# Performance work log

Measured on AMD Instinct MI355X. Metric: run time of the kernel, lower is better.

The kernel has to match this reference:

```python
import jax, jax.numpy as jnp
import numpy as np

LAG = 24      # lag (months of 20 days) in the train window
STEP = 20     # days per rebalancing step
ANNUAL = 252.0


def setup_inputs() -> dict:
    key = jax.random.key(0)
    Y = jax.random.normal(key, (20480, 128), dtype=jnp.float32) * 0.01  # daily returns
    a = jnp.full((1,), 0.997, dtype=jnp.float32)                        # EWMA decay param
    logridge = jnp.full((1,), float(np.log(1e-5)), dtype=jnp.float32)   # log ridge param
    return {"Y": Y, "a": a, "logridge": logridge}


def reference(Y, a, logridge):
    n, p = Y.shape
    W = n // STEP - LAG            # number of rolling windows (1000)
    T = LAG * STEP                 # train window length (480)
    a0 = a[0]
    ridge = jnp.exp(logridge[0])

    # EWMA weights: w_t = a^(T-1-t) (most recent day has weight 1), normalized to sum T
    expo = jnp.arange(T - 1, -1, -1, dtype=Y.dtype)
    w = a0 ** expo
    w = w / w.sum() * T
    wsum = w.sum()
    denom = 1.0 - (w * w).sum() / (T * T)   # bias correction (w**2 / T**2).sum()
    ones_p = jnp.ones((p,), Y.dtype)

    def per_window(j):
        # train: Y[(i-lag)*20 : i*20] with i = j + LAG  ->  rows [j*20, j*20+T)
        Yt = jax.lax.dynamic_slice(Y, (j * STEP, 0), (T, p))
        # test: Y[i*20 : (i+1)*20]
        Yte = jax.lax.dynamic_slice(Y, ((j + LAG) * STEP, 0), (STEP, p))
        mean = (w[:, None] * Yt).sum(axis=0) / wsum          # [p]
        Yc = Yt - mean[None, :]                               # [T, p]
        Sigma = (Yc.T @ (w[:, None] * Yc)) / T / denom        # [p, p] weighted covariance
        lam, U = jnp.linalg.eigh(Sigma)
        Pmat = (U / (ridge + lam)[None, :]) @ U.T             # ridge-shrunk precision
        # GMV weights: P @ 1 / (1' P 1)
        v = Pmat @ ones_p
        wgt = v / (ones_p @ v)
        ret = Yte @ wgt                                       # [STEP] portfolio returns
        e = ret.sum()                                         # cumulative test return
        s = (ret * ret).mean()                                # realized daily variance
        return e, s

    e_all, s_all = jax.vmap(per_window)(jnp.arange(W))
    vol = jnp.sqrt(s_all.mean() * ANNUAL)
    mu = e_all.mean() / STEP * ANNUAL
    sharpe = mu / vol
    return vol, mu, sharpe
```

## Files before the change

kernel.cpp:

```cpp
#include <hip/hip_runtime.h>
#include <math.h>

#define P 128
#define T_WIN 480
#define STEPD 20
#define LAG_W 24
#define NITER 12
#define SEG 64
#define PACK 8448
#define PCHUNK 33

__device__ __forceinline__ int tri_off(int r) {
  const int a = r >> 2, b = r & 3;
  return ((a + 1) * (2 * a + b)) << 2;
}

__device__ __forceinline__ void ewma_consts(float af, double& la, float& Sf, float& denomf) {
  const double a = (double)af;
  la = log(a);
  const double A480 = exp(480.0 * la);
  const double S = (1.0 - A480) / (1.0 - a);
  const double Su2 = (1.0 - A480 * A480) / (1.0 - a * a);
  Sf = (float)S;
  denomf = (float)(1.0 - Su2 / (S * S));
}

__global__ __launch_bounds__(256) void cblocks_kernel(const float* __restrict__ Y,
                                                      const float* __restrict__ aarg,
                                                      float* __restrict__ cvec,
                                                      float* __restrict__ Call, int K) {
  const int k = blockIdx.x;
  const int tid = threadIdx.x;
  const int ti = tid >> 4, tj = tid & 15;
  __shared__ float st[STEPD][P];
  __shared__ float sbwsm[STEPD];
  if (tid < STEPD) {
    const double la = log((double)aarg[0]);
    sbwsm[tid] = (float)exp(0.5 * (double)(STEPD - 1 - tid) * la);
  }
  __syncthreads();
  const float* __restrict__ Yb = Y + (size_t)k * STEPD * P;
  for (int i = tid; i < STEPD * P / 4; i += 256) {
    float4 v = ((const float4*)Yb)[i];
    const float sw = sbwsm[i >> 5];
    v.x *= sw; v.y *= sw; v.z *= sw; v.w *= sw;
    ((float4*)&st[0][0])[i] = v;
  }
  __syncthreads();

  float acc[8][8];
#pragma unroll
  for (int u = 0; u < 8; ++u)
#pragma unroll
    for (int v = 0; v < 8; ++v) acc[u][v] = 0.0f;

#pragma unroll 4
  for (int t = 0; t < STEPD; ++t) {
    float af[8], bf[8];
    *(float4*)(af)     = *(const float4*)&st[t][ti * 4];
    *(float4*)(af + 4) = *(const float4*)&st[t][64 + ti * 4];
    *(float4*)(bf)     = *(const float4*)&st[t][tj * 4];
    *(float4*)(bf + 4) = *(const float4*)&st[t][64 + tj * 4];
#pragma unroll
    for (int u = 0; u < 8; ++u)
#pragma unroll
      for (int v = 0; v < 8; ++v) acc[u][v] += af[u] * bf[v];
  }

  float* __restrict__ Ck = Call + (size_t)k * PACK;
#pragma unroll
  for (int u = 0; u < 8; ++u) {
    const int r = (u < 4) ? (ti * 4 + u) : (64 + ti * 4 + u - 4);
    const int offr = tri_off(r);
    if (tj * 4 <= r) {
      float4 o0;
      o0.x = acc[u][0]; o0.y = acc[u][1]; o0.z = acc[u][2]; o0.w = acc[u][3];
      *(float4*)(Ck + offr + tj * 4) = o0;
    }
    if (64 + tj * 4 <= r) {
      float4 o1;
      o1.x = acc[u][4]; o1.y = acc[u][5]; o1.z = acc[u][6]; o1.w = acc[u][7];
      *(float4*)(Ck + offr + 64 + tj * 4) = o1;
    }
  }
  if (tid < P) {
    float s = 0.0f;
    for (int t = 0; t < STEPD; ++t) s += sbwsm[t] * st[t][tid];
    cvec[(size_t)k * P + tid] = s;
  }
}

__global__ __launch_bounds__(256) void scan_kernel(float* __restrict__ Call,
                                                   const float* __restrict__ aarg) {
  __shared__ float asm_[SEG];
  const int tid = threadIdx.x;
  const int seg = blockIdx.x / PCHUNK;
  const int chunk = blockIdx.x - seg * PCHUNK;
  if (tid < SEG) {
    const double la = log((double)aarg[0]);
    asm_[tid] = (float)exp(-(double)(20 * tid) * la);
  }
  __syncthreads();
  const int e = chunk * 256 + tid;
  float* __restrict__ base = Call + ((size_t)seg * SEG) * PACK + e;
  float g = 0.0f;
#pragma unroll 4
  for (int k = 0; k < SEG; ++k) {
    const float c = base[(size_t)k * PACK];
    g = fmaf(asm_[k], c, g);
    base[(size_t)k * PACK] = g;
  }
}

__global__ __launch_bounds__(128, 2) void window14_kernel(
    const float* __restrict__ Y, const float* __restrict__ aarg,
    const float* __restrict__ logridge, const float* __restrict__ cvec,
    const float* __restrict__ Gall, float* __restrict__ e_all,
    float* __restrict__ s_all, int W) {
  const int bid = blockIdx.x;
  const int q = W >> 3, r8 = W & 7;
  const int xcd = bid & 7, idx = bid >> 3;
  const int j = ((xcd < r8) ? (xcd * (q + 1)) : (r8 * (q + 1) + (xcd - r8) * q)) + idx;

  const int tid = threadIdx.x;
  const int ti = tid >> 4, tj = tid & 15;
  const int lane = tid & 63;
  const int wv = tid >> 6;
  const int rowbase = ti * 16;

  __shared__ float Gsm[PACK];
  __shared__ float rsm[P];
  __shared__ float vsm[P];
  __shared__ float meansm[P];
  __shared__ float coefsm[LAG_W];
  __shared__ float2 gd_wave[2];
  __shared__ float rs_wave[2];
  __shared__ float retd[STEPD];

  double la_d;
  float S, denom;
  ewma_consts(aarg[0], la_d, S, denom);
  const float ridge = expf(logridge[0]);

  if (tid < LAG_W)
    coefsm[tid] = (float)exp((double)(STEPD * (LAG_W - 1 - tid)) * la_d);
  __syncthreads();

  int offR[16];
#pragma unroll
  for (int u = 0; u < 16; ++u) offR[u] = tri_off(rowbase + u);
  int colv[8], offC[8];
#pragma unroll
  for (int v = 0; v < 8; ++v) {
    colv[v] = (v < 4) ? (tj * 4 + v) : (64 + tj * 4 + (v - 4));
    offC[v] = tri_off(colv[v]);
  }

  int mats[3];
  float scls[3];
  int nm = 0;
  {
    const int o1 = j & ~(SEG - 1);
    const int end = j + 23;
    const int b = o1 + SEG;
    const float pA = (float)exp((double)(STEPD * (end - o1)) * la_d);
    if (end < b) {
      mats[nm] = end; scls[nm] = pA; ++nm;
      if (j > o1) { mats[nm] = j - 1; scls[nm] = -pA; ++nm; }
    } else {
      const float pB2 = (float)exp((double)(STEPD * (end - b)) * la_d);
      mats[nm] = b - 1; scls[nm] = pA; ++nm;
      if (j > o1) { mats[nm] = j - 1; scls[nm] = -pA; ++nm; }
      mats[nm] = end; scls[nm] = pB2; ++nm;
    }
  }

  {
    float4* __restrict__ Gsm4 = (float4*)Gsm;
    if (nm == 3) {
      const float cf0 = scls[0], cf1 = scls[1], cf2 = scls[2];
      const float4* __restrict__ G0 = (const float4*)(Gall + (size_t)mats[0] * PACK);
      const float4* __restrict__ G1 = (const float4*)(Gall + (size_t)mats[1] * PACK);
      const float4* __restrict__ G2 = (const float4*)(Gall + (size_t)mats[2] * PACK);
      for (int i = tid; i < PACK / 4; i += 128) {
        const float4 a0 = G0[i];
        const float4 a1 = G1[i];
        const float4 a2 = G2[i];
        float4 o;
        o.x = cf0 * a0.x + cf1 * a1.x + cf2 * a2.x;
        o.y = cf0 * a0.y + cf1 * a1.y + cf2 * a2.y;
        o.z = cf0 * a0.z + cf1 * a1.z + cf2 * a2.z;
        o.w = cf0 * a0.w + cf1 * a1.w + cf2 * a2.w;
        Gsm4[i] = o;
      }
    } else {
      const float cf0 = scls[0];
      const float cf1 = (nm > 1) ? scls[1] : 0.0f;
      const float4* __restrict__ G0 = (const float4*)(Gall + (size_t)mats[0] * PACK);
      const float4* __restrict__ G1 = (const float4*)(Gall + (size_t)mats[(nm > 1) ? 1 : 0] * PACK);
      for (int i = tid; i < PACK / 4; i += 128) {
        const float4 a0 = G0[i];
        const float4 a1 = G1[i];
        float4 o;
        o.x = cf0 * a0.x + cf1 * a1.x;
        o.y = cf0 * a0.y + cf1 * a1.y;
        o.z = cf0 * a0.z + cf1 * a1.z;
        o.w = cf0 * a0.w + cf1 * a1.w;
        Gsm4[i] = o;
      }
    }
  }

  {
    float s = 0.0f;
    for (int m = 0; m < LAG_W; ++m) s += coefsm[m] * cvec[(size_t)(j + m) * P + tid];
    meansm[tid] = s;
    rsm[tid] = 1.0f;
  }
  __syncthreads();

  float acc[16][8];
  {
    const float sc1 = 1.0f / (S * denom);
    const float sc2 = 1.0f / (S * S * denom);
#pragma unroll
    for (int u = 0; u < 16; ++u) {
      const int r = rowbase + u;
      const int offr = offR[u];
      const float mr = meansm[r] * sc2;
#pragma unroll
      for (int v = 0; v < 8; ++v) {
        const int c = colv[v];
        const int idxe = (c <= r) ? (offr + c) : (offC[v] + r);
        float mval = Gsm[idxe] * sc1 - mr * meansm[c];
        if (r == c) mval += ridge;
        acc[u][v] = mval;
      }
    }
  }
  __syncthreads();

  float xo = 0.0f, ro = 1.0f, po = 0.0f, so = 0.0f;
  float gam_old = 1.0f, alp_old = 1.0f;

  for (int it = 0; it < NITER; ++it) {
    const float4 p0 = *(const float4*)&rsm[tj * 4];
    const float4 p1 = *(const float4*)&rsm[64 + tj * 4];
    float pv[8] = {p0.x, p0.y, p0.z, p0.w, p1.x, p1.y, p1.z, p1.w};
    float ap[16];
#pragma unroll
    for (int u = 0; u < 16; ++u) {
      float s = 0.0f;
#pragma unroll
      for (int v = 0; v < 8; ++v) s += acc[u][v] * pv[v];
      ap[u] = s;
    }
#pragma unroll
    for (int m = 1; m <= 8; m <<= 1) {
#pragma unroll
      for (int u = 0; u < 16; ++u) ap[u] += __shfl_xor(ap[u], m);
    }
    float wv_c = ap[0];
#pragma unroll
    for (int u = 1; u < 16; ++u) wv_c = (tj == u) ? ap[u] : wv_c;

    {
      const float4 r0 = *(const float4*)&rsm[rowbase];
      const float4 r1 = *(const float4*)&rsm[rowbase + 4];
      const float4 r2 = *(const float4*)&rsm[rowbase + 8];
      const float4 r3 = *(const float4*)&rsm[rowbase + 12];
      const float rv[16] = {r0.x, r0.y, r0.z, r0.w, r1.x, r1.y, r1.z, r1.w,
                            r2.x, r2.y, r2.z, r2.w, r3.x, r3.y, r3.z, r3.w};
      float gp = 0.0f, dp = 0.0f;
#pragma unroll
      for (int u = 0; u < 16; ++u) {
        gp = fmaf(rv[u], rv[u], gp);
        dp = fmaf(ap[u], rv[u], dp);
      }
      gp += __shfl_down(gp, 16); dp += __shfl_down(dp, 16);
      gp += __shfl_down(gp, 32); dp += __shfl_down(dp, 32);
      if (lane == 0) { gd_wave[wv].x = gp; gd_wave[wv].y = dp; }
    }
    __syncthreads();

    const float gam = gd_wave[0].x + gd_wave[1].x;
    const float del = gd_wave[0].y + gd_wave[1].y;
    float bet, alp;
    if (it == 0) { bet = 0.0f; alp = gam / del; }
    else {
      bet = gam / gam_old;
      alp = gam / (del - bet * gam / alp_old);
    }
    gam_old = gam; alp_old = alp;

    po = ro + bet * po;
    so = wv_c + bet * so;
    xo += alp * po;
    ro -= alp * so;
    rsm[tid] = ro;
    __syncthreads();
  }

  vsm[tid] = xo;
  float sv = xo;
#pragma unroll
  for (int m = 32; m > 0; m >>= 1) sv += __shfl_down(sv, m);
  if (lane == 0) rs_wave[wv] = sv;
  __syncthreads();
  const float sumv = rs_wave[0] + rs_wave[1];

  const float* __restrict__ Yte = Y + (size_t)(j + LAG_W) * STEPD * P;
  for (int d = wv; d < STEPD; d += 2) {
    float pp = Yte[(size_t)d * P + lane] * vsm[lane] +
               Yte[(size_t)d * P + 64 + lane] * vsm[64 + lane];
    for (int off = 32; off > 0; off >>= 1) pp += __shfl_down(pp, off);
    if (lane == 0) retd[d] = pp;
  }
  __syncthreads();

  if (tid == 0) {
    const float invs = 1.0f / sumv;
    float e = 0.0f, s = 0.0f;
#pragma unroll
    for (int d = 0; d < STEPD; ++d) {
      const float rr = retd[d] * invs;
      e += rr; s += rr * rr;
    }
    e_all[j] = e;
    s_all[j] = s * (1.0f / (float)STEPD);
  }
}

__global__ __launch_bounds__(256, 2) void window_fallback(
    const float* __restrict__ Y, const float* __restrict__ aarg,
    const float* __restrict__ logridge, float* __restrict__ e_all,
    float* __restrict__ s_all, int W) {
  const int j = blockIdx.x;
  const int tid = threadIdx.x;
  const int ti = tid >> 4;
  const int tj = tid & 15;

  __shared__ float Msm[P][P + 1];
  __shared__ float wsm[T_WIN];
  __shared__ float swsm[T_WIN];
  __shared__ float meansm[P];
  __shared__ float red[256];
  __shared__ float retd[STEPD];
  __shared__ float zsm[P];
  __shared__ float vsm[P];
  __shared__ float bsm[P];

  float* stage = &Msm[0][0];

  double la;
  float S, denom;
  ewma_consts(aarg[0], la, S, denom);
  for (int t = tid; t < T_WIN; t += 256) {
    const double wn = exp((double)(T_WIN - 1 - t) * la) / (double)S * (double)T_WIN;
    wsm[t] = (float)wn;
    swsm[t] = (float)sqrt(wn);
  }
  if (tid < P) bsm[tid] = 1.0f;
  const float ridge = expf(logridge[0]);
  __syncthreads();

  const float* __restrict__ Ywin = Y + (size_t)j * STEPD * P;
  {
    const int col = tid & 127;
    const int half = tid >> 7;
    float m = 0.0f;
    const int t0 = half * (T_WIN / 2), t1 = t0 + T_WIN / 2;
    for (int t = t0; t < t1; ++t) m += wsm[t] * Ywin[(size_t)t * P + col];
    red[tid] = m;
    __syncthreads();
    if (tid < P) meansm[tid] = (red[tid] + red[tid + 128]) * (1.0f / (float)T_WIN);
    __syncthreads();
  }

  float acc[8][8];
#pragma unroll
  for (int u = 0; u < 8; ++u)
#pragma unroll
    for (int v = 0; v < 8; ++v) acc[u][v] = 0.0f;

  for (int c = 0; c < T_WIN / 32; ++c) {
    __syncthreads();
#pragma unroll
    for (int i = 0; i < 4; ++i) {
      const int idx = i * 1024 + tid * 4;
      float4 v = *(const float4*)(Ywin + (size_t)c * 32 * P + idx);
      const float sw = swsm[c * 32 + (idx >> 7)];
      v.x *= sw; v.y *= sw; v.z *= sw; v.w *= sw;
      *(float4*)(stage + idx) = v;
    }
    __syncthreads();
#pragma unroll 4
    for (int t = 0; t < 32; ++t) {
      const float* rowp = stage + t * P;
      float af[8], bf[8];
      *(float4*)(af) = *(const float4*)(rowp + ti * 8);
      *(float4*)(af + 4) = *(const float4*)(rowp + ti * 8 + 4);
      *(float4*)(bf) = *(const float4*)(rowp + tj * 8);
      *(float4*)(bf + 4) = *(const float4*)(rowp + tj * 8 + 4);
#pragma unroll
      for (int u = 0; u < 8; ++u)
#pragma unroll
        for (int v = 0; v < 8; ++v) acc[u][v] += af[u] * bf[v];
    }
  }
  __syncthreads();

  const float invTd = 1.0f / ((float)T_WIN * denom);
#pragma unroll
  for (int u = 0; u < 8; ++u) {
    const int r = ti * 8 + u;
    const float mr = meansm[r];
#pragma unroll
    for (int v = 0; v < 8; ++v) {
      const int cc = tj * 8 + v;
      float m = (acc[u][v] - (float)T_WIN * mr * meansm[cc]) * invTd;
      if (r == cc) m += ridge;
      Msm[r][cc] = m;
    }
  }
  __syncthreads();

  for (int k = 0; k < P; ++k) {
    const float dkk = Msm[k][k];
    const float sq = sqrtf(dkk);
    const float invd = 1.0f / sq;
    if (tid == 0) Msm[k][k] = sq;
    const int i = k + 1 + tid;
    if (i < P) Msm[i][k] *= invd;
    __syncthreads();
    const int nrem = P - 1 - k;
    for (int ii = ti; ii < nrem; ii += 16) {
      const int ri = k + 1 + ii;
      const float Lik = Msm[ri][k];
      for (int jj = tj; jj < nrem; jj += 16) {
        const int cj = k + 1 + jj;
        Msm[ri][cj] -= Lik * Msm[cj][k];
      }
    }
    __syncthreads();
  }

  for (int k = 0; k < P; ++k) {
    const float zk = bsm[k] / Msm[k][k];
    if (tid == 0) zsm[k] = zk;
    const int i = k + 1 + tid;
    if (i < P) bsm[i] -= Msm[i][k] * zk;
    __syncthreads();
  }
  for (int k = P - 1; k >= 0; --k) {
    const float vk = zsm[k] / Msm[k][k];
    if (tid == 0) vsm[k] = vk;
    if (tid < k) zsm[tid] -= Msm[k][tid] * vk;
    __syncthreads();
  }

  red[tid] = (tid < P) ? vsm[tid] : 0.0f;
  __syncthreads();
  for (int off = 128; off > 0; off >>= 1) {
    if (tid < off) red[tid] += red[tid + off];
    __syncthreads();
  }

  const float* __restrict__ Yte = Y + (size_t)(j + LAG_W) * STEPD * P;
  const int wv = tid >> 6;
  const int lane = tid & 63;
  for (int d = wv; d < STEPD; d += 4) {
    float pp = Yte[(size_t)d * P + lane] * vsm[lane] +
               Yte[(size_t)d * P + 64 + lane] * vsm[64 + lane];
    for (int off = 32; off > 0; off >>= 1) pp += __shfl_down(pp, off);
    if (lane == 0) retd[d] = pp;
  }
  __syncthreads();

  if (tid == 0) {
    const float invs = 1.0f / red[0];
    float e = 0.0f, s = 0.0f;
#pragma unroll
    for (int d = 0; d < STEPD; ++d) {
      const float r = retd[d] * invs;
      e += r;
      s += r * r;
    }
    e_all[j] = e;
    s_all[j] = s * (1.0f / (float)STEPD);
  }
}

__global__ __launch_bounds__(256) void final_kernel(const float* __restrict__ e_all,
                                                    const float* __restrict__ s_all,
                                                    float* __restrict__ out, int W) {
  __shared__ float r1[256], r2[256];
  const int tid = threadIdx.x;
  float e = 0.0f, s = 0.0f;
  for (int i = tid; i < W; i += 256) {
    e += e_all[i];
    s += s_all[i];
  }
  r1[tid] = e;
  r2[tid] = s;
  __syncthreads();
  for (int off = 128; off > 0; off >>= 1) {
    if (tid < off) {
      r1[tid] += r1[tid + off];
      r2[tid] += r2[tid + off];
    }
    __syncthreads();
  }
  if (tid == 0) {
    const float vol = sqrtf(r2[0] / (float)W * 252.0f);
    const float mu = r1[0] / (float)W / (float)STEPD * 252.0f;
    out[0] = vol;
    out[1] = mu;
    out[2] = mu / vol;
  }
}

extern "C" void kernel_launch(void* const* d_in, const int* in_sizes, int n_in,
                              void* d_out, int out_size, void* d_ws, size_t ws_size,
                              hipStream_t stream) {
  const float* Y = (const float*)d_in[0];
  const float* a = (const float*)d_in[1];
  const float* logridge = (const float*)d_in[2];
  float* out = (float*)d_out;

  const int n = in_sizes[0] / P;
  const int K = n / STEPD;
  const int W = K - LAG_W;

  float* ws = (float*)d_ws;
  float* e_all = ws;
  float* s_all = ws + 1024;
  float* cvec = ws + 2048;
  float* Gall = ws + 2048 + (size_t)K * P;

  const size_t need = ((size_t)2048 + (size_t)K * P + (size_t)K * PACK) * sizeof(float);

  if (ws_size >= need && (n % STEPD) == 0 && W > 0 && W <= 1024 && (K % SEG) == 0) {
    cblocks_kernel<<<K, 256, 0, stream>>>(Y, a, cvec, Gall, K);
    scan_kernel<<<(K / SEG) * PCHUNK, 256, 0, stream>>>(Gall, a);
    window14_kernel<<<W, 128, 0, stream>>>(Y, a, logridge, cvec, Gall, e_all, s_all, W);
  } else {
    window_fallback<<<W, 256, 0, stream>>>(Y, a, logridge, e_all, s_all, W);
    final_kernel<<<1, 256, 0, stream>>>(e_all, s_all, out, W);
    return;
  }
  final_kernel<<<1, 256, 0, stream>>>(e_all, s_all, out, W);
}
```

Baseline: 81.10 us.

## Prefix-scan mean vectors alongside covariance blocks and cut eigen iterations

The scan kernel gains extra blocks that run the same EWMA segmented prefix scan over the per-block mean vectors (cvec). This lets each window build its weighted mean from the same one or two scanned matrices and scales it uses for the covariance, instead of a 24-term sum over raw blocks, and it removes the coefsm setup and one barrier. Separately, the iteration count NITER drops from 12 to 10, which cuts iterative solver work at some risk to numerical accuracy.

```diff
diff --git a/kernel.cpp b/kernel.cpp
--- a/kernel.cpp
+++ b/kernel.cpp
@@ -5,7 +5,7 @@
 #define T_WIN 480
 #define STEPD 20
 #define LAG_W 24
-#define NITER 12
+#define NITER 10
 #define SEG 64
 #define PACK 8448
 #define PCHUNK 33
@@ -91,28 +91,47 @@
 }
 
 __global__ __launch_bounds__(256) void scan_kernel(float* __restrict__ Call,
-                                                   const float* __restrict__ aarg) {
+                                                   float* __restrict__ cvec,
+                                                   const float* __restrict__ aarg,
+                                                   int nseg, int gblocks) {
   __shared__ float asm_[SEG];
   const int tid = threadIdx.x;
-  const int seg = blockIdx.x / PCHUNK;
-  const int chunk = blockIdx.x - seg * PCHUNK;
+  const int bid = blockIdx.x;
   if (tid < SEG) {
     const double la = log((double)aarg[0]);
     asm_[tid] = (float)exp(-(double)(20 * tid) * la);
   }
   __syncthreads();
-  const int e = chunk * 256 + tid;
-  float* __restrict__ base = Call + ((size_t)seg * SEG) * PACK + e;
-  float g = 0.0f;
+  if (bid < gblocks) {
+    const int seg = bid / PCHUNK;
+    const int chunk = bid - seg * PCHUNK;
+    const int e = chunk * 256 + tid;
+    float* __restrict__ base = Call + ((size_t)seg * SEG) * PACK + e;
+    float g = 0.0f;
 #pragma unroll 4
-  for (int k = 0; k < SEG; ++k) {
-    const float c = base[(size_t)k * PACK];
-    g = fmaf(asm_[k], c, g);
-    base[(size_t)k * PACK] = g;
-  }
-}
-
-__global__ __launch_bounds__(128, 2) void window14_kernel(
+    for (int k = 0; k < SEG; ++k) {
+      const float c = base[(size_t)k * PACK];
+      g = fmaf(asm_[k], c, g);
+      base[(size_t)k * PACK] = g;
+    }
+  } else {
+    const int chain = (bid - gblocks) * 256 + tid;
+    if (chain < nseg * P) {
+      const int seg = chain >> 7;
+      const int col = chain & (P - 1);
+      float* __restrict__ base = cvec + ((size_t)seg * SEG) * P + col;
+      float g = 0.0f;
+#pragma unroll 4
+      for (int k = 0; k < SEG; ++k) {
+        const float c = base[(size_t)k * P];
+        g = fmaf(asm_[k], c, g);
+        base[(size_t)k * P] = g;
+      }
+    }
+  }
+}
+
+__global__ __launch_bounds__(128, 2) void window15_kernel(
     const float* __restrict__ Y, const float* __restrict__ aarg,
     const float* __restrict__ logridge, const float* __restrict__ cvec,
     const float* __restrict__ Gall, float* __restrict__ e_all,
@@ -132,7 +151,6 @@
   __shared__ float rsm[P];
   __shared__ float vsm[P];
   __shared__ float meansm[P];
-  __shared__ float coefsm[LAG_W];
   __shared__ float2 gd_wave[2];
   __shared__ float rs_wave[2];
   __shared__ float retd[STEPD];
@@ -141,10 +159,6 @@
   float S, denom;
   ewma_consts(aarg[0], la_d, S, denom);
   const float ridge = expf(logridge[0]);
-
-  if (tid < LAG_W)
-    coefsm[tid] = (float)exp((double)(STEPD * (LAG_W - 1 - tid)) * la_d);
-  __syncthreads();
 
   int offR[16];
 #pragma unroll
@@ -213,7 +227,8 @@
 
   {
     float s = 0.0f;
-    for (int m = 0; m < LAG_W; ++m) s += coefsm[m] * cvec[(size_t)(j + m) * P + tid];
+    for (int m = 0; m < nm; ++m)
+      s += scls[m] * cvec[(size_t)mats[m] * P + tid];
     meansm[tid] = s;
     rsm[tid] = 1.0f;
   }
@@ -541,13 +556,14 @@
   const size_t need = ((size_t)2048 + (size_t)K * P + (size_t)K * PACK) * sizeof(float);
 
   if (ws_size >= need && (n % STEPD) == 0 && W > 0 && W <= 1024 && (K % SEG) == 0) {
+    const int nseg = K / SEG;
+    const int gblocks = nseg * PCHUNK;
+    const int cblocks2 = (nseg * P + 255) / 256;
     cblocks_kernel<<<K, 256, 0, stream>>>(Y, a, cvec, Gall, K);
-    scan_kernel<<<(K / SEG) * PCHUNK, 256, 0, stream>>>(Gall, a);
-    window14_kernel<<<W, 128, 0, stream>>>(Y, a, logridge, cvec, Gall, e_all, s_all, W);
+    scan_kernel<<<gblocks + cblocks2, 256, 0, stream>>>(Gall, cvec, a, nseg, gblocks);
+    window15_kernel<<<W, 128, 0, stream>>>(Y, a, logridge, cvec, Gall, e_all, s_all, W);
   } else {
     window_fallback<<<W, 256, 0, stream>>>(Y, a, logridge, e_all, s_all, W);
-    final_kernel<<<1, 256, 0, stream>>>(e_all, s_all, out, W);
-    return;
   }
   final_kernel<<<1, 256, 0, stream>>>(e_all, s_all, out, W);
 }
```

New measurement: 89.13 us. 9.9% more time.
